# Optimization experiments

Hardware: AMD Instinct MI355X
Metric: run time of the kernel (lower is better)

## Reference

```python
import jax, jax.numpy as jnp
import numpy as np

N_NODES = 50000
N_EDGES = 400000
IN_F = 512
HID = 512      # 2 * out_features
OUT_F = 256
N_CELL = 1000
N_DIM = 128
N_SEL = 8192
N_C = 1024


def setup_inputs() -> dict:
    key = jax.random.key(0)
    ks = jax.random.split(key, 16)
    x = jax.random.normal(ks[0], (N_NODES, IN_F), dtype=jnp.float32)
    src = jax.random.randint(ks[1], (N_EDGES,), 0, N_NODES, dtype=jnp.int32)
    dst = jax.random.randint(ks[2], (N_EDGES,), 0, N_NODES, dtype=jnp.int32)
    x_indices = jax.random.randint(ks[3], (N_SEL,), 0, N_NODES, dtype=jnp.int32)
    c_indices = jax.random.randint(ks[4], (N_C,), 0, N_CELL, dtype=jnp.int32)
    s = lambda f: 1.0 / np.sqrt(f)
    W1 = jax.random.normal(ks[5], (IN_F, HID), dtype=jnp.float32) * s(IN_F)
    b1 = jnp.zeros((HID,), jnp.float32)
    W2 = jax.random.normal(ks[6], (HID, HID), dtype=jnp.float32) * s(HID)
    b2 = jnp.zeros((HID,), jnp.float32)
    W3 = jax.random.normal(ks[7], (HID, OUT_F), dtype=jnp.float32) * s(HID)
    b3 = jnp.zeros((OUT_F,), jnp.float32)
    Wp = jax.random.normal(ks[8], (OUT_F, N_DIM), dtype=jnp.float32) * s(OUT_F)
    bp = jnp.zeros((N_DIM,), jnp.float32)
    emb = jax.random.normal(ks[9], (N_CELL, N_DIM), dtype=jnp.float32)
    return {"x": x, "src": src, "dst": dst, "x_indices": x_indices,
            "c_indices": c_indices, "W1": W1, "b1": b1, "W2": W2, "b2": b2,
            "W3": W3, "b3": b3, "Wp": Wp, "bp": bp, "emb": emb}


def _degree_norms(src, dst, n):
    ones = jnp.ones(src.shape[0], jnp.float32)
    deg_out = jax.ops.segment_sum(ones, src, num_segments=n)
    deg_in = jax.ops.segment_sum(ones, dst, num_segments=n)
    ns = jnp.where(deg_out > 0, jax.lax.rsqrt(jnp.maximum(deg_out, 1.0)), 0.0)
    nd = jnp.where(deg_in > 0, jax.lax.rsqrt(jnp.maximum(deg_in, 1.0)), 0.0)
    return ns[:, None], nd[:, None]


def _gconv(h, src, dst, norm_src, norm_dst, W, b, n):
    # DGL GraphConv, norm='both': D_in^{-1/2} A D_out^{-1/2} H W + b
    msg = (h * norm_src)[src]                         # [E, F]
    agg = jax.ops.segment_sum(msg, dst, num_segments=n)
    return (agg * norm_dst) @ W + b


def reference(x, src, dst, x_indices, c_indices, W1, b1, W2, b2, W3, b3, Wp, bp, emb):
    n = x.shape[0]
    ns, nd = _degree_norms(src, dst, n)
    h = jax.nn.relu(_gconv(x, src, dst, ns, nd, W1, b1, n))
    h = jax.nn.relu(_gconv(h, src, dst, ns, nd, W2, b2, n))
    h = jax.nn.relu(_gconv(h, src, dst, ns, nd, W3, b3, n))
    enc = h[x_indices]                                # [N_SEL, OUT_F]
    proj = enc @ Wp + bp                              # Dropout in eval mode = identity
    e = emb[c_indices]                                # [N_C, N_DIM]
    return e @ proj.T                                 # [N_C, N_SEL]
```

## Files before the change

kernel.cpp:

```cpp
#include <hip/hip_runtime.h>

typedef unsigned int u32;
typedef unsigned short u16;

#define N_NODES 50000
#define N_EDGES 400000
#define IN_F 512
#define HID 512
#define OUT_F 256
#define N_CELL 1000
#define N_DIM 128
#define N_SEL 8192
#define N_C 1024
#define MPAD 50176

#define SCAN_B 256
#define SCAN_NB ((N_NODES + SCAN_B - 1) / SCAN_B)

typedef __bf16 bf16x8 __attribute__((ext_vector_type(8)));
typedef float f32x4 __attribute__((ext_vector_type(4)));

__device__ __forceinline__ u16 f2bf(float f) {
    u32 u = __builtin_bit_cast(u32, f);
    u32 r = (u + 0x7fffu + ((u >> 16) & 1u)) >> 16;
    return (u16)r;
}
__device__ __forceinline__ float bf2f(u32 bits16) {
    return __builtin_bit_cast(float, bits16 << 16);
}

__device__ __forceinline__ void async_copy16(const u16* g, u16* l) {
    __builtin_amdgcn_global_load_lds(
        (const __attribute__((address_space(1))) void*)g,
        (__attribute__((address_space(3))) void*)l, 16, 0, 0);
}


__global__ void degrees_kernel(const int* __restrict__ src, const int* __restrict__ dst,
                               int* __restrict__ degO, int* __restrict__ degI) {
    int e = blockIdx.x * 256 + threadIdx.x;
    if (e < N_EDGES) {
        atomicAdd(&degO[src[e]], 1);
        atomicAdd(&degI[dst[e]], 1);
    }
}

__global__ void scan_blocksum_kernel(const int* __restrict__ deg, int* __restrict__ bsum) {
    __shared__ int sh[SCAN_B];
    int i = blockIdx.x * SCAN_B + threadIdx.x;
    int v = (i < N_NODES) ? deg[i] : 0;
    sh[threadIdx.x] = v;
    __syncthreads();
    for (int off = SCAN_B / 2; off > 0; off >>= 1) {
        if (threadIdx.x < off) sh[threadIdx.x] += sh[threadIdx.x + off];
        __syncthreads();
    }
    if (threadIdx.x == 0) bsum[blockIdx.x] = sh[0];
}

__global__ void scan_bsum_kernel(const int* __restrict__ bsum, int* __restrict__ boff) {
    __shared__ int sh[SCAN_B];
    const int t = threadIdx.x;
    int v = (t < SCAN_NB) ? bsum[t] : 0;
    sh[t] = v;
    __syncthreads();
    for (int off = 1; off < SCAN_B; off <<= 1) {
        int u = (t >= off) ? sh[t - off] : 0;
        __syncthreads();
        sh[t] += u;
        __syncthreads();
    }
    if (t < SCAN_NB) boff[t] = sh[t] - v;
}

__global__ void scan_final_kernel(const int* __restrict__ deg, const int* __restrict__ boff,
                                  int* __restrict__ offs) {
    __shared__ int sh[SCAN_B];
    const int t = threadIdx.x;
    int i = blockIdx.x * SCAN_B + t;
    int v = (i < N_NODES) ? deg[i] : 0;
    sh[t] = v;
    __syncthreads();
    for (int off = 1; off < SCAN_B; off <<= 1) {
        int u = (t >= off) ? sh[t - off] : 0;
        __syncthreads();
        sh[t] += u;
        __syncthreads();
    }
    if (i < N_NODES) offs[i] = boff[blockIdx.x] + sh[t] - v;
    if (i == 0) offs[N_NODES] = N_EDGES;
}

__global__ void fill_csr_kernel(const int* __restrict__ src, const int* __restrict__ dst,
                                int* __restrict__ cursor, const int* __restrict__ offs,
                                int* __restrict__ csr) {
    int e = blockIdx.x * 256 + threadIdx.x;
    if (e < N_EDGES) {
        int d = dst[e];
        int slot = atomicAdd(&cursor[d], 1);
        csr[offs[d] + slot] = src[e];
    }
}

__global__ void norms_kernel(const int* __restrict__ degO, const int* __restrict__ degI,
                             float* __restrict__ ns, float* __restrict__ nd) {
    int i = blockIdx.x * 256 + threadIdx.x;
    if (i < N_NODES) {
        ns[i] = degO[i] > 0 ? rsqrtf((float)degO[i]) : 0.f;
        nd[i] = degI[i] > 0 ? rsqrtf((float)degI[i]) : 0.f;
    }
}


__global__ void trans_bf16_kernel(const float* __restrict__ src, u16* __restrict__ dst,
                                  int K, int N) {
    int i = blockIdx.x * 256 + threadIdx.x;
    if (i >= K * N) return;
    int n = i / K, k = i % K;
    dst[i] = f2bf(src[k * N + n]);
}

__global__ void convert_x_kernel(const float* __restrict__ x, u16* __restrict__ xb) {
    int i = blockIdx.x * 256 + threadIdx.x;
    int base = i * 4;
    int m = base >> 9;
    ushort4 o;
    if (m < N_NODES) {
        float4 v = *(const float4*)(x + base);
        o.x = f2bf(v.x); o.y = f2bf(v.y); o.z = f2bf(v.z); o.w = f2bf(v.w);
    } else {
        o = make_ushort4(0, 0, 0, 0);
    }
    *(ushort4*)(xb + base) = o;
}

__global__ void gather_emb_kernel(const float* __restrict__ emb, const int* __restrict__ cidx,
                                  u16* __restrict__ eb) {
    int c = blockIdx.x, f = threadIdx.x;
    eb[c * N_DIM + f] = f2bf(emb[(size_t)cidx[c] * N_DIM + f]);
}

__global__ __launch_bounds__(256, 2) void gemm_bf16_nt(
    const u16* __restrict__ A, const u16* __restrict__ B,
    const int* __restrict__ aidx,
    u16* __restrict__ Cb, float* __restrict__ Cf,
    const float* __restrict__ scale, int nScale,
    const float* __restrict__ bias,
    int N, int K) {
    __shared__ __align__(16) u16 As[2 * 4096];
    __shared__ __align__(16) u16 Bs[2 * 4096];
    const int t = threadIdx.x;
    const int m0 = blockIdx.x * 128, n0 = blockIdx.y * 128;
    const int l = t & 63, w = t >> 6;
    const int wm = (w >> 1) << 6, wn = (w & 1) << 6;
    const int lr = l & 15, quad = l >> 4;

    const int lrow = l >> 2;
    const int kof = (l & 3) << 3;
    const int r0 = w, r1 = w + 4;
    int ar0 = m0 + r0 * 16 + lrow;
    int ar1 = m0 + r1 * 16 + lrow;
    if (aidx) { ar0 = aidx[ar0]; ar1 = aidx[ar1]; }
    const u16* gA0 = A + (size_t)ar0 * K + kof;
    const u16* gA1 = A + (size_t)ar1 * K + kof;
    const u16* gB0 = B + (size_t)(n0 + r0 * 16 + lrow) * K + kof;
    const u16* gB1 = B + (size_t)(n0 + r1 * 16 + lrow) * K + kof;
    u16* lA0 = As + r0 * 512;
    u16* lA1 = As + r1 * 512;
    u16* lB0 = Bs + r0 * 512;
    u16* lB1 = Bs + r1 * 512;

    f32x4 acc[4][4] = {};

    async_copy16(gA0, lA0);
    async_copy16(gA1, lA1);
    async_copy16(gB0, lB0);
    async_copy16(gB1, lB1);

    const int niter = K >> 5;
    for (int it = 0; it < niter; ++it) {
        const int cur = (it & 1) << 12;
        const int nxt = 4096 - cur;
        __syncthreads();
        if (it + 1 < niter) {
            const int ks = (it + 1) << 5;
            async_copy16(gA0 + ks, lA0 + nxt);
            async_copy16(gA1 + ks, lA1 + nxt);
            async_copy16(gB0 + ks, lB0 + nxt);
            async_copy16(gB1 + ks, lB1 + nxt);
        }
        bf16x8 af[4], bg[4];
#pragma unroll
        for (int i = 0; i < 4; ++i)
            af[i] = *(const bf16x8*)&As[cur + (wm + i * 16 + lr) * 32 + quad * 8];
#pragma unroll
        for (int j = 0; j < 4; ++j)
            bg[j] = *(const bf16x8*)&Bs[cur + (wn + j * 16 + lr) * 32 + quad * 8];
#pragma unroll
        for (int i = 0; i < 4; ++i)
#pragma unroll
            for (int j = 0; j < 4; ++j)
                acc[i][j] = __builtin_amdgcn_mfma_f32_16x16x32_bf16(af[i], bg[j], acc[i][j], 0, 0, 0);
    }

#pragma unroll
    for (int i = 0; i < 4; ++i) {
        int rbase = m0 + wm + i * 16 + quad * 4;
#pragma unroll
        for (int j = 0; j < 4; ++j) {
            int col = n0 + wn + j * 16 + lr;
            float bv = bias ? bias[col] : 0.f;
#pragma unroll
            for (int r = 0; r < 4; ++r) {
                int rg = rbase + r;
                float sc = scale ? (rg < nScale ? scale[rg] : 0.f) : 1.f;
                float v = acc[i][j][r] * sc + bv;
                if (Cb) Cb[(size_t)rg * N + col] = f2bf(v);
                else    Cf[(size_t)rg * N + col] = v;
            }
        }
    }
}

template <int W32>
struct AggVec;
template <> struct AggVec<4> { using T = uint4; };
template <> struct AggVec<2> { using T = uint2; };

template <int F>
__global__ __launch_bounds__(256) void aggregate_kernel(
    const u16* __restrict__ T, const int* __restrict__ csr,
    const int* __restrict__ offs, const float* __restrict__ nd,
    const float* __restrict__ bias, u16* __restrict__ H) {
    constexpr int W32 = F / 128;
    using VT = typename AggVec<W32>::T;
    const int t = threadIdx.x, w = t >> 6, l = t & 63;
    const int node = blockIdx.x * 4 + w;
    u32* __restrict__ Hrow = (u32*)H + (size_t)node * (F / 2) + l * W32;
    if (node >= N_NODES) {
        VT z = {};
        *(VT*)Hrow = z;
        return;
    }
    const int s0 = __builtin_amdgcn_readfirstlane(offs[node]);
    const int s1 = __builtin_amdgcn_readfirstlane(offs[node + 1]);
    const u32* __restrict__ Tb = (const u32*)T + l * W32;

    float acc[4][2 * W32];
#pragma unroll
    for (int c = 0; c < 4; ++c)
#pragma unroll
        for (int j = 0; j < 2 * W32; ++j) acc[c][j] = 0.f;

    int e = s0;
    for (; e + 8 <= s1; e += 8) {
        int si[8];
#pragma unroll
        for (int c = 0; c < 8; ++c) si[c] = csr[e + c];
        VT v[8];
#pragma unroll
        for (int c = 0; c < 8; ++c)
            v[c] = *(const VT*)(Tb + (size_t)si[c] * (F / 2));
#pragma unroll
        for (int c = 0; c < 8; ++c) {
            const u32* vv = (const u32*)&v[c];
#pragma unroll
            for (int j = 0; j < W32; ++j) {
                acc[c & 3][2 * j] += bf2f(vv[j] & 0xffffu);
                acc[c & 3][2 * j + 1] += bf2f(vv[j] >> 16);
            }
        }
    }
    for (; e + 4 <= s1; e += 4) {
        int si[4];
#pragma unroll
        for (int c = 0; c < 4; ++c) si[c] = csr[e + c];
        VT v[4];
#pragma unroll
        for (int c = 0; c < 4; ++c)
            v[c] = *(const VT*)(Tb + (size_t)si[c] * (F / 2));
#pragma unroll
        for (int c = 0; c < 4; ++c) {
            const u32* vv = (const u32*)&v[c];
#pragma unroll
            for (int j = 0; j < W32; ++j) {
                acc[c][2 * j] += bf2f(vv[j] & 0xffffu);
                acc[c][2 * j + 1] += bf2f(vv[j] >> 16);
            }
        }
    }
    for (; e < s1; ++e) {
        int s = csr[e];
        VT v = *(const VT*)(Tb + (size_t)s * (F / 2));
        const u32* vv = (const u32*)&v;
#pragma unroll
        for (int j = 0; j < W32; ++j) {
            acc[0][2 * j] += bf2f(vv[j] & 0xffffu);
            acc[0][2 * j + 1] += bf2f(vv[j] >> 16);
        }
    }

    const float ndv = nd[node];
    u32 ow[W32];
#pragma unroll
    for (int j = 0; j < W32; ++j) {
        float a0 = acc[0][2 * j] + acc[1][2 * j] + acc[2][2 * j] + acc[3][2 * j];
        float a1 = acc[0][2 * j + 1] + acc[1][2 * j + 1] + acc[2][2 * j + 1] + acc[3][2 * j + 1];
        float r0 = fmaxf(fmaf(a0, ndv, bias[l * 2 * W32 + 2 * j]), 0.f);
        float r1 = fmaxf(fmaf(a1, ndv, bias[l * 2 * W32 + 2 * j + 1]), 0.f);
        ow[j] = (u32)f2bf(r0) | ((u32)f2bf(r1) << 16);
    }
    VT o;
    u32* op = (u32*)&o;
#pragma unroll
    for (int j = 0; j < W32; ++j) op[j] = ow[j];
    *(VT*)Hrow = o;
}


extern "C" void kernel_launch(void* const* d_in, const int* in_sizes, int n_in,
                              void* d_out, int out_size, void* d_ws, size_t ws_size,
                              hipStream_t stream) {
    const float* x   = (const float*)d_in[0];
    const int*   src = (const int*)d_in[1];
    const int*   dst = (const int*)d_in[2];
    const int*   xidx= (const int*)d_in[3];
    const int*   cidx= (const int*)d_in[4];
    const float* W1  = (const float*)d_in[5];
    const float* b1  = (const float*)d_in[6];
    const float* W2  = (const float*)d_in[7];
    const float* b2  = (const float*)d_in[8];
    const float* W3  = (const float*)d_in[9];
    const float* b3  = (const float*)d_in[10];
    const float* Wp  = (const float*)d_in[11];
    const float* bp  = (const float*)d_in[12];
    const float* emb = (const float*)d_in[13];
    float* out = (float*)d_out;

    char* p = (char*)d_ws;
    auto alloc = [&](size_t bytes) {
        char* r = p;
        p += (bytes + 255) & ~(size_t)255;
        return r;
    };
    u16* T    = (u16*)alloc((size_t)MPAD * 512 * 2);
    u16* HX   = (u16*)alloc((size_t)MPAD * 512 * 2);
    u16* W1T  = (u16*)alloc((size_t)512 * 512 * 2);
    u16* W2T  = (u16*)alloc((size_t)512 * 512 * 2);
    u16* W3T  = (u16*)alloc((size_t)256 * 512 * 2);
    u16* WpT  = (u16*)alloc((size_t)128 * 256 * 2);
    u16* projb= (u16*)alloc((size_t)N_SEL * N_DIM * 2);
    u16* eb   = (u16*)alloc((size_t)N_C * N_DIM * 2);
    int* degO   = (int*)alloc(N_NODES * 4);
    int* degI   = (int*)alloc(N_NODES * 4);
    int* cursor = (int*)alloc(N_NODES * 4);
    int* offs   = (int*)alloc((N_NODES + 1) * 4);
    float* ns   = (float*)alloc(N_NODES * 4);
    float* nd   = (float*)alloc(N_NODES * 4);
    int* csr    = (int*)alloc(N_EDGES * 4);
    int* bsum   = (int*)alloc(SCAN_NB * 4);
    int* boff   = (int*)alloc(SCAN_NB * 4);
    if ((size_t)(p - (char*)d_ws) > ws_size) return;

    hipMemsetAsync(degO, 0, (size_t)((char*)offs - (char*)degO), stream);
    degrees_kernel<<<(N_EDGES + 255) / 256, 256, 0, stream>>>(src, dst, degO, degI);
    scan_blocksum_kernel<<<SCAN_NB, SCAN_B, 0, stream>>>(degI, bsum);
    scan_bsum_kernel<<<1, SCAN_B, 0, stream>>>(bsum, boff);
    scan_final_kernel<<<SCAN_NB, SCAN_B, 0, stream>>>(degI, boff, offs);
    fill_csr_kernel<<<(N_EDGES + 255) / 256, 256, 0, stream>>>(src, dst, cursor, offs, csr);
    norms_kernel<<<(N_NODES + 255) / 256, 256, 0, stream>>>(degO, degI, ns, nd);

    trans_bf16_kernel<<<(512 * 512) / 256, 256, 0, stream>>>(W1, W1T, 512, 512);
    trans_bf16_kernel<<<(512 * 512) / 256, 256, 0, stream>>>(W2, W2T, 512, 512);
    trans_bf16_kernel<<<(512 * 256) / 256, 256, 0, stream>>>(W3, W3T, 512, 256);
    trans_bf16_kernel<<<(256 * 128) / 256, 256, 0, stream>>>(Wp, WpT, 256, 128);
    convert_x_kernel<<<(MPAD * 512 / 4) / 256, 256, 0, stream>>>(x, HX);
    gather_emb_kernel<<<N_C, N_DIM, 0, stream>>>(emb, cidx, eb);

    gemm_bf16_nt<<<dim3(MPAD / 128, 512 / 128), 256, 0, stream>>>(
        HX, W1T, nullptr, T, nullptr, ns, N_NODES, nullptr, 512, 512);
    aggregate_kernel<512><<<MPAD / 4, 256, 0, stream>>>(T, csr, offs, nd, b1, HX);
    gemm_bf16_nt<<<dim3(MPAD / 128, 512 / 128), 256, 0, stream>>>(
        HX, W2T, nullptr, T, nullptr, ns, N_NODES, nullptr, 512, 512);
    aggregate_kernel<512><<<MPAD / 4, 256, 0, stream>>>(T, csr, offs, nd, b2, HX);
    gemm_bf16_nt<<<dim3(MPAD / 128, 256 / 128), 256, 0, stream>>>(
        HX, W3T, nullptr, T, nullptr, ns, N_NODES, nullptr, 256, 512);
    aggregate_kernel<256><<<MPAD / 4, 256, 0, stream>>>(T, csr, offs, nd, b3, HX);

    gemm_bf16_nt<<<dim3(N_SEL / 128, 1), 256, 0, stream>>>(
        HX, WpT, xidx, projb, nullptr, nullptr, 0, bp, N_DIM, 256);
    gemm_bf16_nt<<<dim3(N_C / 128, N_SEL / 128), 256, 0, stream>>>(
        eb, projb, nullptr, nullptr, out, nullptr, 0, nullptr, N_SEL, N_DIM);
}
```

Measured before the change: 597.8 us.

## Deepen GEMM LDS pipeline to four stages with explicit vmcnt waits and XOR swizzle

The bf16 GEMM moves from a double-buffered LDS pipeline to a 4-slot ring with three tiles in flight, using explicit s_waitcnt vmcnt counts and a raw barrier in place of __syncthreads. It also XOR-swizzles the k-chunk offset in both the global-to-LDS copy and the fragment reads to cut LDS bank conflicts. The aim is to hide global load latency and speed up shared-memory reads. LDS use doubles to 64KB per block, which may reduce occupancy under launch_bounds(256,2), and the hand-written wait counts rely on the async copy issuing exactly four vm ops per stage.

```diff
diff --git a/kernel.cpp b/kernel.cpp
--- a/kernel.cpp
+++ b/kernel.cpp
@@ -147,8 +147,8 @@
     const float* __restrict__ scale, int nScale,
     const float* __restrict__ bias,
     int N, int K) {
-    __shared__ __align__(16) u16 As[2 * 4096];
-    __shared__ __align__(16) u16 Bs[2 * 4096];
+    __shared__ __align__(16) u16 As[4 * 4096];
+    __shared__ __align__(16) u16 Bs[4 * 4096];
     const int t = threadIdx.x;
     const int m0 = blockIdx.x * 128, n0 = blockIdx.y * 128;
     const int l = t & 63, w = t >> 6;
@@ -156,7 +156,7 @@
     const int lr = l & 15, quad = l >> 4;
 
     const int lrow = l >> 2;
-    const int kof = (l & 3) << 3;
+    const int kof = (((l & 3) ^ ((l >> 3) & 3)) << 3);
     const int r0 = w, r1 = w + 4;
     int ar0 = m0 + r0 * 16 + lrow;
     int ar1 = m0 + r1 * 16 + lrow;
@@ -172,30 +172,39 @@
 
     f32x4 acc[4][4] = {};
 
-    async_copy16(gA0, lA0);
-    async_copy16(gA1, lA1);
-    async_copy16(gB0, lB0);
-    async_copy16(gB1, lB1);
-
     const int niter = K >> 5;
+
+    auto stage = [&](int j) {
+        const int ks = j << 5;
+        const int bo = (j & 3) << 12;
+        async_copy16(gA0 + ks, lA0 + bo);
+        async_copy16(gA1 + ks, lA1 + bo);
+        async_copy16(gB0 + ks, lB0 + bo);
+        async_copy16(gB1 + ks, lB1 + bo);
+    };
+
+    stage(0);
+    if (niter > 1) stage(1);
+    if (niter > 2) stage(2);
+
+    const int qoff = ((quad ^ ((l >> 1) & 3)) << 3);
+
     for (int it = 0; it < niter; ++it) {
-        const int cur = (it & 1) << 12;
-        const int nxt = 4096 - cur;
-        __syncthreads();
-        if (it + 1 < niter) {
-            const int ks = (it + 1) << 5;
-            async_copy16(gA0 + ks, lA0 + nxt);
-            async_copy16(gA1 + ks, lA1 + nxt);
-            async_copy16(gB0 + ks, lB0 + nxt);
-            async_copy16(gB1 + ks, lB1 + nxt);
-        }
+        const int rem = niter - 1 - it;
+        if (rem >= 2)      asm volatile("s_waitcnt vmcnt(8)" ::: "memory");
+        else if (rem == 1) asm volatile("s_waitcnt vmcnt(4)" ::: "memory");
+        else               asm volatile("s_waitcnt vmcnt(0)" ::: "memory");
+        __builtin_amdgcn_s_barrier();
+        __builtin_amdgcn_sched_barrier(0);
+        if (it + 3 < niter) stage(it + 3);
+        const int cur = (it & 3) << 12;
         bf16x8 af[4], bg[4];
 #pragma unroll
         for (int i = 0; i < 4; ++i)
-            af[i] = *(const bf16x8*)&As[cur + (wm + i * 16 + lr) * 32 + quad * 8];
+            af[i] = *(const bf16x8*)&As[cur + (wm + i * 16 + lr) * 32 + qoff];
 #pragma unroll
         for (int j = 0; j < 4; ++j)
-            bg[j] = *(const bf16x8*)&Bs[cur + (wn + j * 16 + lr) * 32 + quad * 8];
+            bg[j] = *(const bf16x8*)&Bs[cur + (wn + j * 16 + lr) * 32 + qoff];
 #pragma unroll
         for (int i = 0; i < 4; ++i)
 #pragma unroll
```

New measurement: 669.9 us. 1.12x slower.

## Add B-panel-resident GEMM for GCN layers and swizzle LDS in generic GEMM

Applied to the files above, without the earlier changes.

Adds a new GEMM kernel for the three per-layer feature transforms. Each block loads a full 64-column slice of the transposed weight matrix (all of K=512) into LDS once, with an XOR swizzle. It then streams A rows directly from global memory into registers, software-prefetching one k-step ahead, for two 256-row M tiles. Blocks are mapped XCD-aware so blocks that share an A panel stay on the same XCD's L2. Separately, the generic GEMM gets an XOR swizzle on LDS writes and reads to cut bank conflicts. The trade-offs are higher register pressure, 64KB of LDS per block, and A reads with no LDS reuse.

```diff
diff --git a/kernel.cpp b/kernel.cpp
--- a/kernel.cpp
+++ b/kernel.cpp
@@ -138,6 +138,95 @@
                                   u16* __restrict__ eb) {
     int c = blockIdx.x, f = threadIdx.x;
     eb[c * N_DIM + f] = f2bf(emb[(size_t)cidx[c] * N_DIM + f]);
+}
+
+template <int NX>
+__global__ __launch_bounds__(512, 4) void gemm_bpanel(
+    const u16* __restrict__ A, const u16* __restrict__ B,
+    u16* __restrict__ C, const float* __restrict__ scale, int nScale) {
+    constexpr int K = 512;
+    constexpr int BN = 64;
+    constexpr int NF = BN / 32;
+    constexpr int N = NX * BN;
+    __shared__ __align__(16) u16 Bs[BN * K];
+
+    const int g = blockIdx.x;
+    const int xcd = g & 7, idx = g >> 3;
+    const int x = idx % NX, yq = idx / NX;
+    const int y = xcd + (yq << 3);
+    if (y >= 98) return;
+    const int n0p = x * BN;
+
+    const int t = threadIdx.x;
+    const int l = t & 63, w = t >> 6;
+    const int lr = l & 15, quad = l >> 4;
+    const int wm = (w >> 1) << 6;
+    const int wn = (w & 1) * (BN / 2);
+
+#pragma unroll
+    for (int r = 0; r < 8; ++r) {
+        int lin = r * 512 + w * 64 + l;
+        int col = lin >> 6, chl = lin & 63;
+        int c = chl ^ (col & 7);
+        async_copy16(B + (size_t)(n0p + col) * K + c * 8,
+                     Bs + ((r * 512 + w * 64) << 3));
+    }
+    __syncthreads();
+
+    const int xorv = lr & 7;
+    const u16* bbase = Bs + (wn + lr) * K;
+
+    for (int u = 0; u < 2; ++u) {
+        const int m0 = (y + 98 * u) << 8;
+        const u16* ap = A + (size_t)(m0 + wm + lr) * K + quad * 8;
+        f32x4 acc[4][NF] = {};
+        bf16x8 a_n[4], b_n[NF];
+#pragma unroll
+        for (int i = 0; i < 4; ++i) a_n[i] = *(const bf16x8*)(ap + i * 16 * K);
+#pragma unroll
+        for (int j = 0; j < NF; ++j)
+            b_n[j] = *(const bf16x8*)(bbase + j * 16 * K + ((quad ^ xorv) << 3));
+#pragma unroll
+        for (int ks = 0; ks < K / 32; ++ks) {
+            bf16x8 a_c[4], b_c[NF];
+#pragma unroll
+            for (int i = 0; i < 4; ++i) a_c[i] = a_n[i];
+#pragma unroll
+            for (int j = 0; j < NF; ++j) b_c[j] = b_n[j];
+            if (ks + 1 < K / 32) {
+                const int ko = (ks + 1) << 5;
+                const int chb = ((ks + 1) << 2) + quad;
+#pragma unroll
+                for (int i = 0; i < 4; ++i)
+                    a_n[i] = *(const bf16x8*)(ap + i * 16 * K + ko);
+#pragma unroll
+                for (int j = 0; j < NF; ++j)
+                    b_n[j] = *(const bf16x8*)(bbase + j * 16 * K + ((chb ^ xorv) << 3));
+            }
+#pragma unroll
+            for (int i = 0; i < 4; ++i)
+#pragma unroll
+                for (int j = 0; j < NF; ++j)
+                    acc[i][j] = __builtin_amdgcn_mfma_f32_16x16x32_bf16(a_c[i], b_c[j], acc[i][j], 0, 0, 0);
+        }
+#pragma unroll
+        for (int i = 0; i < 4; ++i) {
+            int rbase = m0 + wm + i * 16 + quad * 4;
+            float sc[4];
+#pragma unroll
+            for (int r = 0; r < 4; ++r) {
+                int rg = rbase + r;
+                sc[r] = scale ? (rg < nScale ? scale[rg] : 0.f) : 1.f;
+            }
+#pragma unroll
+            for (int j = 0; j < NF; ++j) {
+                int col = n0p + wn + j * 16 + lr;
+#pragma unroll
+                for (int r = 0; r < 4; ++r)
+                    C[(size_t)(rbase + r) * N + col] = f2bf(acc[i][j][r] * sc[r]);
+            }
+        }
+    }
 }
 
 __global__ __launch_bounds__(256, 2) void gemm_bf16_nt(
@@ -156,7 +245,7 @@
     const int lr = l & 15, quad = l >> 4;
 
     const int lrow = l >> 2;
-    const int kof = (l & 3) << 3;
+    const int kof = (((l & 3) ^ ((l >> 3) & 3)) << 3);
     const int r0 = w, r1 = w + 4;
     int ar0 = m0 + r0 * 16 + lrow;
     int ar1 = m0 + r1 * 16 + lrow;
@@ -177,6 +266,8 @@
     async_copy16(gB0, lB0);
     async_copy16(gB1, lB1);
 
+    const int qoff = ((quad ^ ((l >> 1) & 3)) << 3);
+
     const int niter = K >> 5;
     for (int it = 0; it < niter; ++it) {
         const int cur = (it & 1) << 12;
@@ -192,10 +283,10 @@
         bf16x8 af[4], bg[4];
 #pragma unroll
         for (int i = 0; i < 4; ++i)
-            af[i] = *(const bf16x8*)&As[cur + (wm + i * 16 + lr) * 32 + quad * 8];
+            af[i] = *(const bf16x8*)&As[cur + (wm + i * 16 + lr) * 32 + qoff];
 #pragma unroll
         for (int j = 0; j < 4; ++j)
-            bg[j] = *(const bf16x8*)&Bs[cur + (wn + j * 16 + lr) * 32 + quad * 8];
+            bg[j] = *(const bf16x8*)&Bs[cur + (wn + j * 16 + lr) * 32 + qoff];
 #pragma unroll
         for (int i = 0; i < 4; ++i)
 #pragma unroll
@@ -377,14 +468,14 @@
     convert_x_kernel<<<(MPAD * 512 / 4) / 256, 256, 0, stream>>>(x, HX);
     gather_emb_kernel<<<N_C, N_DIM, 0, stream>>>(emb, cidx, eb);
 
-    gemm_bf16_nt<<<dim3(MPAD / 128, 512 / 128), 256, 0, stream>>>(
-        HX, W1T, nullptr, T, nullptr, ns, N_NODES, nullptr, 512, 512);
+    const int grid8 = 8 * 13 * 8;
+    const int grid4 = 8 * 13 * 4;
+
+    gemm_bpanel<8><<<grid8, 512, 0, stream>>>(HX, W1T, T, ns, N_NODES);
     aggregate_kernel<512><<<MPAD / 4, 256, 0, stream>>>(T, csr, offs, nd, b1, HX);
-    gemm_bf16_nt<<<dim3(MPAD / 128, 512 / 128), 256, 0, stream>>>(
-        HX, W2T, nullptr, T, nullptr, ns, N_NODES, nullptr, 512, 512);
+    gemm_bpanel<8><<<grid8, 512, 0, stream>>>(HX, W2T, T, ns, N_NODES);
     aggregate_kernel<512><<<MPAD / 4, 256, 0, stream>>>(T, csr, offs, nd, b2, HX);
-    gemm_bf16_nt<<<dim3(MPAD / 128, 256 / 128), 256, 0, stream>>>(
-        HX, W3T, nullptr, T, nullptr, ns, N_NODES, nullptr, 256, 512);
+    gemm_bpanel<4><<<grid4, 512, 0, stream>>>(HX, W3T, T, ns, N_NODES);
     aggregate_kernel<256><<<MPAD / 4, 256, 0, stream>>>(T, csr, offs, nd, b3, HX);
 
     gemm_bf16_nt<<<dim3(N_SEL / 128, 1), 256, 0, stream>>>(
```

Result: slower. 809.8 us (+35.5%).
